# Kernel optimization log

Hardware: AMD Instinct MI355X
Metric: run time of the kernel (lower is better)

The kernel has to match this reference:

```python
import jax, jax.numpy as jnp
import numpy as np

INP, OUP, KSIZE, STRIDE = 256, 256, 3, 1
M, G = 2, 2
INP_GAP = max(16, INP // 16)  # 16
PAD = KSIZE // 2


def setup_inputs() -> dict:
    key = jax.random.key(0)
    k1, k2, k3, k4, k5 = jax.random.split(key, 5)
    B, H, W = 32, 28, 28
    x = jax.random.normal(k1, (B, INP, H, W), dtype=jnp.float32)
    x_gap = jax.random.normal(k2, (B, INP_GAP, 1, 1), dtype=jnp.float32)
    # wn_fc1: Conv2d(INP_GAP, M*OUP, 1, bias=True) -> dense [M*OUP, INP_GAP]
    w1 = jax.random.normal(k3, (M * OUP, INP_GAP), dtype=jnp.float32) * 0.1
    b1 = jax.random.normal(k4, (M * OUP,), dtype=jnp.float32) * 0.1
    # wn_fc2: grouped 1x1 conv, groups = G*OUP, 1 in-channel per group
    # -> weight is effectively a vector of length OUP*INP*KSIZE*KSIZE
    w2 = jax.random.normal(k5, (OUP * INP * KSIZE * KSIZE,), dtype=jnp.float32) * 0.05
    return {"x": x, "x_gap": x_gap, "w1": w1, "b1": b1, "w2": w2}


def reference(x, x_gap, w1, b1, w2):
    B, _, H, W = x.shape
    # fc1 (1x1 conv on [B, INP_GAP, 1, 1]) + sigmoid -> [B, M*OUP]
    h = jax.nn.sigmoid(jnp.einsum('bi,oi->bo', x_gap[:, :, 0, 0], w1) + b1)
    # fc2: groups = G*OUP, one input channel per group, INP*K*K/G outputs per group
    per = INP * KSIZE * KSIZE // G
    # [B, G*OUP, per] -> per-sample kernels [B*OUP, INP, K, K]
    wk = (w2.reshape(G * OUP, per) * h[:, :, None]).reshape(B * OUP, INP, KSIZE, KSIZE)
    # batched dynamic conv via feature_group_count = B
    y = jax.lax.conv_general_dilated(
        x.reshape(1, B * INP, H, W), wk,
        window_strides=(STRIDE, STRIDE),
        padding=[(PAD, PAD), (PAD, PAD)],
        dimension_numbers=('NCHW', 'OIHW', 'NCHW'),
        feature_group_count=B)
    return y.reshape(B, OUP, y.shape[2], y.shape[3])
```

## Files before the change

kernel.cpp:

```cpp
#include <hip/hip_runtime.h>
#include <hip/hip_bf16.h>

typedef __attribute__((ext_vector_type(8))) short bf16x8;
typedef __attribute__((ext_vector_type(4))) float f32x4;

#define NB 32
#define NO 256
#define XS_BYTES (6 * 30 * 512)

static __device__ __forceinline__ void gld16(const void* g, void* l) {
    __builtin_amdgcn_global_load_lds(
        (const __attribute__((address_space(1))) void*)g,
        (__attribute__((address_space(3))) void*)l, 16, 0, 0);
}

__global__ void prep_kernel(const float* __restrict__ w2, __hip_bfloat16* __restrict__ wrt,
                            const float* __restrict__ x, __hip_bfloat16* __restrict__ xp) {
    if (blockIdx.x < 288) {
        int idx = blockIdx.x * 256 + threadIdx.x;
        int kcol = idx & 15;
        int klo = (idx >> 4) & 3;
        int mf = (idx >> 6) & 3;
        int mw = (idx >> 8) & 3;
        int kw2 = (idx >> 10) & 1;
        int s = idx >> 11;
        int tap = s >> 2;
        int ic = s & 3;
        int o = mw * 64 + mf * 16 + kcol;
        int ch = kw2 * 128 + ic * 32 + klo * 8;
        const float* src = w2 + (size_t)o * 2304 + (size_t)ch * 9 + tap;
        union { bf16x8 v; __hip_bfloat16 e[8]; } u;
#pragma unroll
        for (int e = 0; e < 8; ++e) u.e[e] = __float2bfloat16(src[e * 9]);
        *(bf16x8*)((short*)wrt + (size_t)idx * 8) = u.v;
        return;
    }
    __shared__ float tile[64][29];
    int blk = blockIdx.x - 288;
    int icnk = blk & 3;
    int t = blk >> 2;
    int pr = t % 30;
    int b = t / 30;
    int i0 = icnk * 64;
    __hip_bfloat16* dst = xp + ((size_t)(b * 30 + pr) * 30) * 256 + i0;
    const bf16x8 z = (bf16x8){0, 0, 0, 0, 0, 0, 0, 0};
    if (pr == 0 || pr == 29) {
        for (int e = threadIdx.x; e < 30 * 8; e += 256) {
            int q = e >> 3, part = e & 7;
            *(bf16x8*)((short*)(dst + (size_t)q * 256) + part * 8) = z;
        }
        return;
    }
    int p = pr - 1;
    for (int e = threadIdx.x; e < 64 * 28; e += 256) {
        int ii = e / 28, q = e % 28;
        tile[ii][q] = x[((b * 256 + i0 + ii) * 28 + p) * 28 + q];
    }
    __syncthreads();
    for (int e = threadIdx.x; e < 28 * 64; e += 256) {
        int q = e >> 6, ii = e & 63;
        dst[(size_t)(q + 1) * 256 + ii] = __float2bfloat16(tile[ii][q]);
    }
    if (threadIdx.x < 16) {
        int col = (threadIdx.x >> 3) * 29, part = threadIdx.x & 7;
        *(bf16x8*)((short*)(dst + (size_t)col * 256) + part * 8) = z;
    }
}

#define MM(A_, B_, mf_, nf_) \
    acc[mf_][nf_] = __builtin_amdgcn_mfma_f32_16x16x32_bf16(A_, B_, acc[mf_][nf_], 0, 0, 0);

#define CL_H1(A0, A1, A2, A3, B0, B1, B2, B3)                           \
    __builtin_amdgcn_s_setprio(1);                                      \
    MM(A0, B0, 0, 0) MM(A1, B0, 1, 0) MM(A2, B0, 2, 0) MM(A3, B0, 3, 0) \
    MM(A0, B1, 0, 1) MM(A1, B1, 1, 1) MM(A2, B1, 2, 1) MM(A3, B1, 3, 1) \
    MM(A0, B2, 0, 2) MM(A1, B2, 1, 2) MM(A2, B2, 2, 2) MM(A3, B2, 3, 2) \
    MM(A0, B3, 0, 3) MM(A1, B3, 1, 3) MM(A2, B3, 2, 3) MM(A3, B3, 3, 3) \
    __builtin_amdgcn_s_setprio(0);
#define CL_H2(A0, A1, A2, A3, B4, B5, B6)                               \
    __builtin_amdgcn_s_setprio(1);                                      \
    MM(A0, B4, 0, 4) MM(A1, B4, 1, 4) MM(A2, B4, 2, 4) MM(A3, B4, 3, 4) \
    MM(A0, B5, 0, 5) MM(A1, B5, 1, 5) MM(A2, B5, 2, 5) MM(A3, B5, 3, 5) \
    MM(A0, B6, 0, 6) MM(A1, B6, 1, 6) MM(A2, B6, 2, 6) MM(A3, B6, 3, 6) \
    __builtin_amdgcn_s_setprio(0);

#define LOADB(D0, D1, D2, D3, D4, D5, D6, XO)                                  \
    D0 = *(const bf16x8*)(Xs + ((u[0] ^ ((kk[0] & 7u) << 4)) ^ (XO)));         \
    D1 = *(const bf16x8*)(Xs + ((u[1] ^ ((kk[1] & 7u) << 4)) ^ (XO)));         \
    D2 = *(const bf16x8*)(Xs + ((u[2] ^ ((kk[2] & 7u) << 4)) ^ (XO)));         \
    D3 = *(const bf16x8*)(Xs + ((u[3] ^ ((kk[3] & 7u) << 4)) ^ (XO)));         \
    D4 = *(const bf16x8*)(Xs + ((u[4] ^ ((kk[4] & 7u) << 4)) ^ (XO)));         \
    D5 = *(const bf16x8*)(Xs + ((u[5] ^ ((kk[5] & 7u) << 4)) ^ (XO)));         \
    D6 = *(const bf16x8*)(Xs + ((u[6] ^ ((kk[6] & 7u) << 4)) ^ (XO)));

#define PHASE_E(BUFOFF, XON)                                                  \
    {                                                                         \
        CL_H1(aA0, aA1, aA2, aA3, bA0, bA1, bA2, bA3)                         \
        asm volatile("s_waitcnt vmcnt(4)" ::: "memory");                      \
        aB0 = *(const bf16x8*)(AbR + (BUFOFF));                               \
        aB1 = *(const bf16x8*)(AbR + (BUFOFF) + 1024);                        \
        aB2 = *(const bf16x8*)(AbR + (BUFOFF) + 2048);                        \
        aB3 = *(const bf16x8*)(AbR + (BUFOFF) + 3072);                        \
        gld16(pG, AbW + (BUFOFF));                                            \
        gld16(pG + 1024, AbW + (BUFOFF) + 1024);                              \
        gld16(pG + 2048, AbW + (BUFOFF) + 2048);                              \
        gld16(pG + 3072, AbW + (BUFOFF) + 3072);                              \
        pG += 32768;                                                          \
        LOADB(bB0, bB1, bB2, bB3, bB4, bB5, bB6, XON)                         \
        __builtin_amdgcn_sched_barrier(0);                                    \
        CL_H2(aA0, aA1, aA2, aA3, bA4, bA5, bA6)                              \
    }
#define PHASE_O(BUFOFF, XON)                                                  \
    {                                                                         \
        CL_H1(aB0, aB1, aB2, aB3, bB0, bB1, bB2, bB3)                         \
        asm volatile("s_waitcnt vmcnt(4)" ::: "memory");                      \
        aA0 = *(const bf16x8*)(AbR + (BUFOFF));                               \
        aA1 = *(const bf16x8*)(AbR + (BUFOFF) + 1024);                        \
        aA2 = *(const bf16x8*)(AbR + (BUFOFF) + 2048);                        \
        aA3 = *(const bf16x8*)(AbR + (BUFOFF) + 3072);                        \
        gld16(pG, AbW + (BUFOFF));                                            \
        gld16(pG + 1024, AbW + (BUFOFF) + 1024);                              \
        gld16(pG + 2048, AbW + (BUFOFF) + 2048);                              \
        gld16(pG + 3072, AbW + (BUFOFF) + 3072);                              \
        pG += 32768;                                                          \
        LOADB(bA0, bA1, bA2, bA3, bA4, bA5, bA6, XON)                         \
        __builtin_amdgcn_sched_barrier(0);                                    \
        CL_H2(aB0, aB1, aB2, aB3, bB4, bB5, bB6)                              \
    }

__global__ __launch_bounds__(512, 2) void conv_kernel(
    const __hip_bfloat16* __restrict__ xp, const __hip_bfloat16* __restrict__ wrt,
    const float* __restrict__ xg, const float* __restrict__ w1,
    const float* __restrict__ b1, float* __restrict__ out) {
    __shared__ __align__(16) char Xs[XS_BYTES];
    __shared__ __align__(16) char Ab[8 * 2 * 4096];
    __shared__ float hsm[512];
    const int bid = blockIdx.x;
    const int v = (bid & 7) * 28 + (bid >> 3);
    const int b = v / 7;
    const int nt = v - b * 7;
    const int tid = threadIdx.x;
    const int lane = tid & 63;
    const int wv = tid >> 6;
    const int mw = wv & 3;
    const int kw2 = wv >> 2;
    const int kcol = lane & 15;
    const int klo = lane >> 4;

    const char* wrtc = (const char*)wrt;
    char* AbW = Ab + wv * 8192;
    const char* AbR = Ab + wv * 8192 + lane * 16;
    const char* pG = wrtc + wv * 4096 + lane * 16;

    gld16(pG, AbW);
    gld16(pG + 1024, AbW + 1024);
    gld16(pG + 2048, AbW + 2048);
    gld16(pG + 3072, AbW + 3072);
    pG += 32768;
    gld16(pG, AbW + 4096);
    gld16(pG + 1024, AbW + 4096 + 1024);
    gld16(pG + 2048, AbW + 4096 + 2048);
    gld16(pG + 3072, AbW + 4096 + 3072);
    pG += 32768;

    {
        float s = b1[tid];
        const float* g = xg + b * 16;
        const float* w = w1 + tid * 16;
#pragma unroll
        for (int c = 0; c < 16; ++c) s += g[c] * w[c];
        hsm[tid] = 1.0f / (1.0f + expf(-s));
    }

    {
        const char* src = (const char*)(xp + ((size_t)b * 900 + nt * 120) * 256);
        for (int c = tid; c < 5760; c += 512) {
            int sp = c >> 5, w = c & 31;
            int rr = sp / 30;
            int qq = sp - rr * 30;
            int key = (qq + 4 * rr) & 7;
            *(bf16x8*)(Xs + sp * 512 + ((w ^ key) << 4)) = *(const bf16x8*)(src + (size_t)c * 16);
        }
    }
    __syncthreads();

    unsigned u[7], kk[7];
#pragma unroll
    for (int nf = 0; nf < 7; ++nf) {
        int n = nf * 16 + kcol;
        int r0 = n / 28;
        int q0 = n - r0 * 28;
        u[nf] = (unsigned)((r0 * 30 + q0) * 512 + (klo << 4));
        kk[nf] = (unsigned)(q0 + 4 * r0);
    }
    const unsigned xo0 = (unsigned)((kw2 * 4 + 0) << 6);
    const unsigned xo1 = (unsigned)((kw2 * 4 + 1) << 6);
    const unsigned xo2 = (unsigned)((kw2 * 4 + 2) << 6);
    const unsigned xo3 = (unsigned)((kw2 * 4 + 3) << 6);

    f32x4 acc[4][7];
#pragma unroll
    for (int mf = 0; mf < 4; ++mf)
#pragma unroll
        for (int nf = 0; nf < 7; ++nf) acc[mf][nf] = (f32x4){0.f, 0.f, 0.f, 0.f};

    bf16x8 aA0, aA1, aA2, aA3, aB0, aB1, aB2, aB3;
    bf16x8 bA0, bA1, bA2, bA3, bA4, bA5, bA6;
    bf16x8 bB0, bB1, bB2, bB3, bB4, bB5, bB6;

    aA0 = *(const bf16x8*)(AbR);
    aA1 = *(const bf16x8*)(AbR + 1024);
    aA2 = *(const bf16x8*)(AbR + 2048);
    aA3 = *(const bf16x8*)(AbR + 3072);
    gld16(pG, AbW);
    gld16(pG + 1024, AbW + 1024);
    gld16(pG + 2048, AbW + 2048);
    gld16(pG + 3072, AbW + 3072);
    pG += 32768;
    LOADB(bA0, bA1, bA2, bA3, bA4, bA5, bA6, xo0)

    for (int tap = 0; tap < 9; ++tap) {
        PHASE_E(4096, xo1)
        PHASE_O(0, xo2)
        PHASE_E(4096, xo3)
        if (tap < 8) {
            const int cross = (tap == 2 || tap == 5);
            const unsigned da = cross ? 28u * 512u : 512u;
            const unsigned dk = cross ? 2u : 1u;
#pragma unroll
            for (int nf = 0; nf < 7; ++nf) { u[nf] += da; kk[nf] += dk; }
        }
        PHASE_O(0, xo0)
    }

    __syncthreads();
    float* Xf = (float*)Xs;
#pragma unroll
    for (int r2 = 0; r2 < 2; ++r2) {
        if (kw2 == 1) {
#pragma unroll
            for (int mfi = 0; mfi < 2; ++mfi) {
                const int mf = r2 * 2 + mfi;
#pragma unroll
                for (int nf = 0; nf < 7; ++nf) {
#pragma unroll
                    for (int rr = 0; rr < 4; ++rr) {
                        int o = mw * 64 + mf * 16 + klo * 4 + rr;
                        int idx = (((mw * 2 + mfi) * 7 + nf) * 4 + rr) * 64 + lane;
                        Xf[idx] = hsm[2 * o + 1] * acc[mf][nf][rr];
                    }
                }
            }
        }
        __syncthreads();
        if (kw2 == 0) {
#pragma unroll
            for (int mfi = 0; mfi < 2; ++mfi) {
                const int mf = r2 * 2 + mfi;
#pragma unroll
                for (int nf = 0; nf < 7; ++nf) {
#pragma unroll
                    for (int rr = 0; rr < 4; ++rr) {
                        int o = mw * 64 + mf * 16 + klo * 4 + rr;
                        int idx = (((mw * 2 + mfi) * 7 + nf) * 4 + rr) * 64 + lane;
                        float y = hsm[2 * o] * acc[mf][nf][rr] + Xf[idx];
                        out[((size_t)b * NO + o) * 784 + nt * 112 + nf * 16 + kcol] = y;
                    }
                }
            }
        }
        __syncthreads();
    }
}

extern "C" void kernel_launch(void* const* d_in, const int* in_sizes, int n_in,
                              void* d_out, int out_size, void* d_ws, size_t ws_size,
                              hipStream_t stream) {
    const float* x = (const float*)d_in[0];
    const float* xg = (const float*)d_in[1];
    const float* w1 = (const float*)d_in[2];
    const float* b1 = (const float*)d_in[3];
    const float* w2 = (const float*)d_in[4];
    float* out = (float*)d_out;

    char* ws = (char*)d_ws;
    __hip_bfloat16* wrt = (__hip_bfloat16*)ws;
    __hip_bfloat16* xp = (__hip_bfloat16*)(ws + 1179648);

    prep_kernel<<<288 + NB * 30 * 4, 256, 0, stream>>>(w2, wrt, x, xp);
    conv_kernel<<<224, 512, 0, stream>>>(xp, wrt, xg, w1, b1, out);
}
```

Before: 49.72 us.

## Fuse input padding and bf16 transpose into conv kernel load stage

The separate prep pass that padded and transposed x from NCHW fp32 into an NHWC bf16 workspace is removed. The conv kernel now reads fp32 x directly with 16-byte loads, converts each value to bf16 and scatters it into the swizzled shared-memory tile, zeroing the halo itself. This drops a global write and re-read of the padded activation tensor, but the shared-memory stores become 2-byte scattered writes and neighbouring blocks re-read the overlapping halo rows of x.

```diff
diff --git a/kernel.cpp b/kernel.cpp
--- a/kernel.cpp
+++ b/kernel.cpp
@@ -14,57 +14,23 @@
         (__attribute__((address_space(3))) void*)l, 16, 0, 0);
 }
 
-__global__ void prep_kernel(const float* __restrict__ w2, __hip_bfloat16* __restrict__ wrt,
-                            const float* __restrict__ x, __hip_bfloat16* __restrict__ xp) {
-    if (blockIdx.x < 288) {
-        int idx = blockIdx.x * 256 + threadIdx.x;
-        int kcol = idx & 15;
-        int klo = (idx >> 4) & 3;
-        int mf = (idx >> 6) & 3;
-        int mw = (idx >> 8) & 3;
-        int kw2 = (idx >> 10) & 1;
-        int s = idx >> 11;
-        int tap = s >> 2;
-        int ic = s & 3;
-        int o = mw * 64 + mf * 16 + kcol;
-        int ch = kw2 * 128 + ic * 32 + klo * 8;
-        const float* src = w2 + (size_t)o * 2304 + (size_t)ch * 9 + tap;
-        union { bf16x8 v; __hip_bfloat16 e[8]; } u;
-#pragma unroll
-        for (int e = 0; e < 8; ++e) u.e[e] = __float2bfloat16(src[e * 9]);
-        *(bf16x8*)((short*)wrt + (size_t)idx * 8) = u.v;
-        return;
-    }
-    __shared__ float tile[64][29];
-    int blk = blockIdx.x - 288;
-    int icnk = blk & 3;
-    int t = blk >> 2;
-    int pr = t % 30;
-    int b = t / 30;
-    int i0 = icnk * 64;
-    __hip_bfloat16* dst = xp + ((size_t)(b * 30 + pr) * 30) * 256 + i0;
-    const bf16x8 z = (bf16x8){0, 0, 0, 0, 0, 0, 0, 0};
-    if (pr == 0 || pr == 29) {
-        for (int e = threadIdx.x; e < 30 * 8; e += 256) {
-            int q = e >> 3, part = e & 7;
-            *(bf16x8*)((short*)(dst + (size_t)q * 256) + part * 8) = z;
-        }
-        return;
-    }
-    int p = pr - 1;
-    for (int e = threadIdx.x; e < 64 * 28; e += 256) {
-        int ii = e / 28, q = e % 28;
-        tile[ii][q] = x[((b * 256 + i0 + ii) * 28 + p) * 28 + q];
-    }
-    __syncthreads();
-    for (int e = threadIdx.x; e < 28 * 64; e += 256) {
-        int q = e >> 6, ii = e & 63;
-        dst[(size_t)(q + 1) * 256 + ii] = __float2bfloat16(tile[ii][q]);
-    }
-    if (threadIdx.x < 16) {
-        int col = (threadIdx.x >> 3) * 29, part = threadIdx.x & 7;
-        *(bf16x8*)((short*)(dst + (size_t)col * 256) + part * 8) = z;
-    }
+__global__ void prep_kernel(const float* __restrict__ w2, __hip_bfloat16* __restrict__ wrt) {
+    int idx = blockIdx.x * 256 + threadIdx.x;
+    int kcol = idx & 15;
+    int klo = (idx >> 4) & 3;
+    int mf = (idx >> 6) & 3;
+    int mw = (idx >> 8) & 3;
+    int kw2 = (idx >> 10) & 1;
+    int s = idx >> 11;
+    int tap = s >> 2;
+    int ic = s & 3;
+    int o = mw * 64 + mf * 16 + kcol;
+    int ch = kw2 * 128 + ic * 32 + klo * 8;
+    const float* src = w2 + (size_t)o * 2304 + (size_t)ch * 9 + tap;
+    union { bf16x8 v; __hip_bfloat16 e[8]; } u;
+#pragma unroll
+    for (int e = 0; e < 8; ++e) u.e[e] = __float2bfloat16(src[e * 9]);
+    *(bf16x8*)((short*)wrt + (size_t)idx * 8) = u.v;
 }
 
 #define MM(A_, B_, mf_, nf_) \
@@ -129,7 +95,7 @@
     }
 
 __global__ __launch_bounds__(512, 2) void conv_kernel(
-    const __hip_bfloat16* __restrict__ xp, const __hip_bfloat16* __restrict__ wrt,
+    const float* __restrict__ x, const __hip_bfloat16* __restrict__ wrt,
     const float* __restrict__ xg, const float* __restrict__ w1,
     const float* __restrict__ b1, float* __restrict__ out) {
     __shared__ __align__(16) char Xs[XS_BYTES];
@@ -173,13 +139,43 @@
     }
 
     {
-        const char* src = (const char*)(xp + ((size_t)b * 900 + nt * 120) * 256);
-        for (int c = tid; c < 5760; c += 512) {
-            int sp = c >> 5, w = c & 31;
-            int rr = sp / 30;
-            int qq = sp - rr * 30;
-            int key = (qq + 4 * rr) & 7;
-            *(bf16x8*)(Xs + sp * 512 + ((w ^ key) << 4)) = *(const bf16x8*)(src + (size_t)c * 16);
+        const bf16x8 z = (bf16x8){0, 0, 0, 0, 0, 0, 0, 0};
+        for (int e = tid; e < 6 * 2 * 32; e += 512) {
+            int w = e & 31;
+            int t2 = e >> 5;
+            int row = t2 >> 1;
+            int col = (t2 & 1) ? 29 : 0;
+            *(bf16x8*)(Xs + (row * 30 + col) * 512 + w * 16) = z;
+        }
+        if (nt == 0) {
+            for (int e = tid; e < 30 * 32; e += 512)
+                *(bf16x8*)(Xs + (e >> 5) * 512 + (e & 31) * 16) = z;
+        }
+        if (nt == 6) {
+            for (int e = tid; e < 30 * 32; e += 512)
+                *(bf16x8*)(Xs + (150 + (e >> 5)) * 512 + (e & 31) * 16) = z;
+        }
+        const int p0 = nt * 4 - 1;
+        const float* xb = x + (size_t)b * 256 * 784;
+        for (int e = tid; e < 1536 * 7; e += 512) {
+            int c4 = e % 7;
+            int pair = e / 7;
+            int ch = pair & 255;
+            int row = pair >> 8;
+            int p = p0 + row;
+            if (p >= 0 && p < 28) {
+                f32x4 val = *(const f32x4*)(xb + ((size_t)ch * 28 + p) * 28 + 4 * c4);
+                int w = ch >> 3;
+                int bi = (ch & 7) * 2;
+                int spb = row * 30 + 4 * c4 + 1;
+#pragma unroll
+                for (int k = 0; k < 4; ++k) {
+                    int sp = spb + k;
+                    int key = ((4 * c4 + 1 + k) + 4 * row) & 7;
+                    *(__hip_bfloat16*)(Xs + sp * 512 + (((w ^ key) << 4) | bi)) =
+                        __float2bfloat16(val[k]);
+                }
+            }
         }
     }
     __syncthreads();
@@ -285,8 +281,7 @@
 
     char* ws = (char*)d_ws;
     __hip_bfloat16* wrt = (__hip_bfloat16*)ws;
-    __hip_bfloat16* xp = (__hip_bfloat16*)(ws + 1179648);
-
-    prep_kernel<<<288 + NB * 30 * 4, 256, 0, stream>>>(w2, wrt, x, xp);
-    conv_kernel<<<224, 512, 0, stream>>>(xp, wrt, xg, w1, b1, out);
-}
+
+    prep_kernel<<<288, 256, 0, stream>>>(w2, wrt);
+    conv_kernel<<<224, 512, 0, stream>>>(x, wrt, xg, w1, b1, out);
+}
```

After: 46.10 us. 7.3% less time.
